# Kernel tuning notes

Hardware: AMD Instinct MI355X
Metric: run time of the kernel (lower is better)

Reference implementation:

```python
import jax, jax.numpy as jnp
import numpy as np

E = 8          # num_experts
H = 2048       # hidden_size
D = 4096       # expert_dim
R = 8          # lora rank
SCALE = 16.0 / 8.0  # lora_alpha / r
T = 2048       # tokens per expert


def setup_inputs() -> dict:
    key = jax.random.key(0)
    ks = jax.random.split(key, 7)
    s = lambda *shape: 1.0 / np.sqrt(shape[-1])
    hidden_states = jax.random.normal(ks[0], (E * T, H), dtype=jnp.float32)
    # base weights (nn.Linear convention: [out, in]) stacked over experts
    W_gu = jax.random.normal(ks[1], (E, 2 * D, H), dtype=jnp.float32) * s(H)
    W_d = jax.random.normal(ks[2], (E, H, D), dtype=jnp.float32) * s(D)
    # LoRA factors: A [r, in] (kaiming-ish), B [out, r] (zeros in training init;
    # use small random here so the delta path is exercised)
    A_gu = jax.random.normal(ks[3], (E, R, H), dtype=jnp.float32) * s(H)
    B_gu = jax.random.normal(ks[4], (E, 2 * D, R), dtype=jnp.float32) * 0.01
    A_d = jax.random.normal(ks[5], (E, R, D), dtype=jnp.float32) * s(D)
    B_d = jax.random.normal(ks[6], (E, H, R), dtype=jnp.float32) * 0.01
    return {"hidden_states": hidden_states, "W_gu": W_gu, "A_gu": A_gu,
            "B_gu": B_gu, "W_d": W_d, "A_d": A_d, "B_d": B_d}


def _lora_linear(x, W, A, B):
    # x: [e, t, in]; W: [e, out, in]; A: [e, r, in]; B: [e, out, r]
    base = jnp.einsum('eti,eoi->eto', x, W)
    low = jnp.einsum('eti,eri->etr', x, A)        # skinny projection
    delta = jnp.einsum('etr,eor->eto', low, B)
    return base + SCALE * delta


def reference(hidden_states, W_gu, A_gu, B_gu, W_d, A_d, B_d):
    x = hidden_states.reshape(E, -1, H)           # [E, T, H]
    gate_up = _lora_linear(x, W_gu, A_gu, B_gu)   # [E, T, 2D]
    gate, up = gate_up[..., :D], gate_up[..., D:]
    h = up * jax.nn.silu(gate)                    # SwiGLU [E, T, D]
    out = _lora_linear(h, W_d, A_d, B_d)          # [E, T, H]
    return out.reshape(-1, H)
```

## Files before the change

### kernel.cpp

```cpp
#include <hip/hip_runtime.h>
#include <hip/hip_bf16.h>

#define E_ 8
#define H_ 2048
#define D_ 4096
#define R_ 8
#define T_ 2048
#define TWO_D_ 8192
#define SCALE_ 2.0f

typedef __attribute__((ext_vector_type(8))) short short8;
typedef __attribute__((ext_vector_type(4))) float f32x4;

__device__ __forceinline__ unsigned short f2bf(float f) {
  union { float f; unsigned u; } c; c.f = f;
  unsigned u = c.u + 0x7fffu + ((c.u >> 16) & 1u);
  return (unsigned short)(u >> 16);
}

__device__ __forceinline__ void gl16(const void* g, void* l) {
  __builtin_amdgcn_global_load_lds(
      (const __attribute__((address_space(1))) void*)g,
      (__attribute__((address_space(3))) void*)l, 16, 0, 0);
}

__device__ __forceinline__ int lds_off(int rr, int ks, int lq) {
  return (((rr >> 5) & 3) << 13) | (((rr >> 7) & 1) << 12) | ((rr & 31) << 7) | (ks << 6) | (lq << 4);
}

__global__ __launch_bounds__(256) void k_pre(const float* __restrict__ x,
                                             unsigned short* __restrict__ xb,
                                             const float* __restrict__ Wgu,
                                             const float* __restrict__ Agu,
                                             const float* __restrict__ Bgu,
                                             unsigned short* __restrict__ wgub,
                                             const float* __restrict__ Wd,
                                             const float* __restrict__ Ad,
                                             const float* __restrict__ Bd,
                                             unsigned short* __restrict__ wdb) {
  const int NB_X = 1024, NB_GU = 8192;
  int bb = blockIdx.x, tid = threadIdx.x;
  if (bb < NB_X) {
    const long n = (long)E_ * T_ * H_;
    long i = ((long)bb * 256 + tid) * 8;
    const long stride = (long)NB_X * 256 * 8;
    for (; i < n; i += stride) {
      f32x4 a = *(const f32x4*)(x + i);
      f32x4 b = *(const f32x4*)(x + i + 4);
      ushort4 lo, hi;
      lo.x=f2bf(a[0]); lo.y=f2bf(a[1]); lo.z=f2bf(a[2]); lo.w=f2bf(a[3]);
      hi.x=f2bf(b[0]); hi.y=f2bf(b[1]); hi.z=f2bf(b[2]); hi.w=f2bf(b[3]);
      *(ushort4*)(xb + i) = lo;
      *(ushort4*)(xb + i + 4) = hi;
    }
  } else if (bb < NB_X + NB_GU) {
    int b2 = bb - NB_X;
    int e = b2 >> 10;
    int o8 = (b2 & 1023) * 8;
    int c = tid * 8;
    f32x4 a0[8], a1[8];
    #pragma unroll
    for (int r = 0; r < 8; ++r) {
      const float* ap = Agu + ((long)e * R_ + r) * H_ + c;
      a0[r] = *(const f32x4*)ap;
      a1[r] = *(const f32x4*)(ap + 4);
    }
    #pragma unroll
    for (int o = 0; o < 8; ++o) {
      long row = (long)e * TWO_D_ + o8 + o;
      const float* bp = Bgu + row * R_;
      const float* wp = Wgu + row * (long)H_ + c;
      f32x4 w0 = *(const f32x4*)wp;
      f32x4 w1 = *(const f32x4*)(wp + 4);
      #pragma unroll
      for (int r = 0; r < 8; ++r) {
        float s = SCALE_ * bp[r];
        w0 += s * a0[r];
        w1 += s * a1[r];
      }
      ushort4 lo, hi;
      lo.x=f2bf(w0[0]); lo.y=f2bf(w0[1]); lo.z=f2bf(w0[2]); lo.w=f2bf(w0[3]);
      hi.x=f2bf(w1[0]); hi.y=f2bf(w1[1]); hi.z=f2bf(w1[2]); hi.w=f2bf(w1[3]);
      unsigned short* op = wgub + row * (long)H_ + c;
      *(ushort4*)op = lo;
      *(ushort4*)(op + 4) = hi;
    }
  } else {
    int b2 = bb - NB_X - NB_GU;
    int e = b2 >> 9;
    int rem = b2 & 511;
    int h8 = (rem >> 1) * 8;
    int c = (rem & 1) * 2048 + tid * 8;
    f32x4 a0[8], a1[8];
    #pragma unroll
    for (int r = 0; r < 8; ++r) {
      const float* ap = Ad + ((long)e * R_ + r) * D_ + c;
      a0[r] = *(const f32x4*)ap;
      a1[r] = *(const f32x4*)(ap + 4);
    }
    #pragma unroll
    for (int o = 0; o < 8; ++o) {
      long row = (long)e * H_ + h8 + o;
      const float* bp = Bd + row * R_;
      const float* wp = Wd + row * (long)D_ + c;
      f32x4 w0 = *(const f32x4*)wp;
      f32x4 w1 = *(const f32x4*)(wp + 4);
      #pragma unroll
      for (int r = 0; r < 8; ++r) {
        float s = SCALE_ * bp[r];
        w0 += s * a0[r];
        w1 += s * a1[r];
      }
      ushort4 lo, hi;
      lo.x=f2bf(w0[0]); lo.y=f2bf(w0[1]); lo.z=f2bf(w0[2]); lo.w=f2bf(w0[3]);
      hi.x=f2bf(w1[0]); hi.y=f2bf(w1[1]); hi.z=f2bf(w1[2]); hi.w=f2bf(w1[3]);
      unsigned short* op = wdb + row * (long)D_ + c;
      *(ushort4*)op = lo;
      *(ushort4*)(op + 4) = hi;
    }
  }
}

__global__ __launch_bounds__(512, 2) void k_gemm1_8p(
    const unsigned short* __restrict__ Xb, const unsigned short* __restrict__ Wb,
    unsigned short* __restrict__ Hout) {
  __shared__ __align__(16) char lds[131072];

  const int MT = T_ / 256, NT = D_ / 128;
  int b = blockIdx.x;
  int cpx = (int)gridDim.x >> 3;
  int swz = (b & 7) * cpx + (b >> 3);
  int e  = swz / (MT * NT);
  int r0 = swz % (MT * NT);
  int nt = r0 / MT, mt = r0 % MT;

  int tid = threadIdx.x, lane = tid & 63;
  int wid = tid >> 6, wm = wid >> 2, wn = wid & 3;
  int lrow = lane & 15, lq = lane >> 4;
  int X4 = (lrow & 7) << 4;
  const int NKT = H_ / 64;

  unsigned ro = (unsigned)tid * 16;
  unsigned so = ro ^ (((ro >> 7) & 7u) << 4);
  int sh = (so >> 12) & 1, sr = (so >> 7) & 31, sc = (so & 127) >> 1;
  const unsigned short* pA[4]; const unsigned short* pB[4];
  #pragma unroll
  for (int q = 0; q < 4; ++q) {
    long arow = (long)e * T_ + mt * 256 + sh * 128 + q * 32 + sr;
    pA[q] = Xb + arow * H_ + sc;
    long wrow = sh ? ((long)e * TWO_D_ + D_ + nt * 128 + q * 32 + sr)
                   : ((long)e * TWO_D_ +      nt * 128 + q * 32 + sr);
    pB[q] = Wb + wrow * (long)H_ + sc;
  }
  auto SA = [&](int d, int q) { gl16(pA[q], lds + d * 32768 + q * 8192 + ro); pA[q] += 64; };
  auto SB = [&](int d, int q) { gl16(pB[q], lds + 65536 + d * 32768 + q * 8192 + ro); pB[q] += 64; };

  f32x4 accg[2][8] = {}, accu[2][8] = {};
  short8 BG[2][2], BU[2][2], af[2][2];

  SA(0,0); SB(0,0); SA(0,1); SB(0,1); SA(0,2); SB(0,2); SA(0,3); SB(0,3);
  SA(1,0); SB(1,0); SA(1,1); SB(1,1); SA(1,2); SB(1,2);
  asm volatile("s_waitcnt vmcnt(6)" ::: "memory");
  __builtin_amdgcn_s_barrier();

  int rbA = wm * 128 + lrow;
  for (int t = 0; t < NKT; ++t) {
    int d = t & 1;
    const char* Ab = lds + d * 32768;
    const char* Bb = lds + 65536 + d * 32768;

#define G1_MFMA(q)                                                                   \
    __builtin_amdgcn_s_setprio(1);                                                   \
    _Pragma("unroll") for (int m2 = 0; m2 < 2; ++m2)                                 \
      _Pragma("unroll") for (int ks = 0; ks < 2; ++ks)                               \
        _Pragma("unroll") for (int nj = 0; nj < 2; ++nj) {                           \
          accg[nj][(q)*2+m2] = __builtin_amdgcn_mfma_f32_16x16x32_bf16(              \
              BG[nj][ks], af[m2][ks], accg[nj][(q)*2+m2], 0, 0, 0);                  \
          accu[nj][(q)*2+m2] = __builtin_amdgcn_mfma_f32_16x16x32_bf16(              \
              BU[nj][ks], af[m2][ks], accu[nj][(q)*2+m2], 0, 0, 0);                  \
        }                                                                            \
    __builtin_amdgcn_s_setprio(0);

#define G1_LDA(q)                                                                    \
    _Pragma("unroll") for (int m2 = 0; m2 < 2; ++m2)                                 \
      _Pragma("unroll") for (int ks = 0; ks < 2; ++ks)                               \
        af[m2][ks] = *(const short8*)(Ab + (lds_off(rbA + ((q)*2+m2)*16, ks, lq) ^ X4));

#define G1_SYNC()                                                                    \
    __builtin_amdgcn_s_barrier();                                                    \
    asm volatile("s_waitcnt lgkmcnt(0)" ::: "memory");

    #pragma unroll
    for (int nj = 0; nj < 2; ++nj)
      #pragma unroll
      for (int ks = 0; ks < 2; ++ks) {
        int rg = wn * 32 + nj * 16 + lrow;
        BG[nj][ks] = *(const short8*)(Bb + (lds_off(rg, ks, lq) ^ X4));
        BU[nj][ks] = *(const short8*)(Bb + (lds_off(rg + 128, ks, lq) ^ X4));
      }
    G1_LDA(0);
    if (t + 1 < NKT) { SA(d ^ 1, 3); SB(d ^ 1, 3); }
    G1_SYNC();
    G1_MFMA(0);
    __builtin_amdgcn_s_barrier();
    G1_LDA(1);
    if (t + 2 < NKT) { SA(d, 0); SB(d, 0); }
    G1_SYNC();
    G1_MFMA(1);
    __builtin_amdgcn_s_barrier();
    G1_LDA(2);
    if (t + 2 < NKT) { SA(d, 1); SB(d, 1); }
    G1_SYNC();
    G1_MFMA(2);
    __builtin_amdgcn_s_barrier();
    G1_LDA(3);
    if (t + 2 < NKT) {
      SA(d, 2); SB(d, 2);
      asm volatile("s_waitcnt vmcnt(6)" ::: "memory");
    } else {
      asm volatile("s_waitcnt vmcnt(0)" ::: "memory");
    }
    G1_SYNC();
    G1_MFMA(3);
    __builtin_amdgcn_s_barrier();
  }

  __syncthreads();
  unsigned short* sT = (unsigned short*)(lds + 32768);
  #pragma unroll
  for (int mi = 0; mi < 8; ++mi) {
    int tl = rbA + mi * 16;
    #pragma unroll
    for (int nj = 0; nj < 2; ++nj) {
      int cb = wn * 32 + nj * 16 + lq * 4;
      ushort4 o;
      #pragma unroll
      for (int j = 0; j < 4; ++j) {
        float gate = accg[nj][mi][j];
        float up   = accu[nj][mi][j];
        float hh = up * (gate / (1.f + __expf(-gate)));
        (&o.x)[j] = f2bf(hh);
      }
      *(ushort4*)(sT + tl * 136 + cb) = o;
    }
  }
  __syncthreads();
  {
    long base = ((long)e * T_ + mt * 256) * D_ + nt * 128;
    int rr2 = tid >> 4, cc2 = (tid & 15) * 8;
    #pragma unroll
    for (int p = 0; p < 8; ++p) {
      int r = p * 32 + rr2;
      short8 v = *(const short8*)(sT + r * 136 + cc2);
      *(short8*)(Hout + base + (long)r * D_ + cc2) = v;
    }
  }
}

__global__ __launch_bounds__(512, 2) void k_gemm2_8p(
    const unsigned short* __restrict__ Hin, const unsigned short* __restrict__ Wdb,
    float* __restrict__ Out) {
  __shared__ __align__(16) char lds[131072];

  const int MT = T_ / 256, NT = H_ / 256;
  int b = blockIdx.x;
  int cpx = (int)gridDim.x >> 3;
  int swz = (b & 7) * cpx + (b >> 3);
  int e  = swz / (MT * NT);
  int r0 = swz % (MT * NT);
  int nt = r0 / MT, mt = r0 % MT;

  int tid = threadIdx.x, lane = tid & 63;
  int wid = tid >> 6, wm = wid >> 2, wn = wid & 3;
  int lrow = lane & 15, lq = lane >> 4;
  int X4 = (lrow & 7) << 4;
  const int NKT = D_ / 64;

  unsigned ro = (unsigned)tid * 16;
  unsigned so = ro ^ (((ro >> 7) & 7u) << 4);
  int sh = (so >> 12) & 1, sr = (so >> 7) & 31, sc = (so & 127) >> 1;
  const unsigned short* pA[4]; const unsigned short* pB[4];
  #pragma unroll
  for (int q = 0; q < 4; ++q) {
    long arow = (long)e * T_ + mt * 256 + sh * 128 + q * 32 + sr;
    pA[q] = Hin + arow * D_ + sc;
    long wrow = (long)e * H_ + nt * 256 + sh * 128 + q * 32 + sr;
    pB[q] = Wdb + wrow * (long)D_ + sc;
  }
  auto SA = [&](int d, int q) { gl16(pA[q], lds + d * 32768 + q * 8192 + ro); pA[q] += 64; };
  auto SB = [&](int d, int q) { gl16(pB[q], lds + 65536 + d * 32768 + q * 8192 + ro); pB[q] += 64; };

  f32x4 acc[8][4] = {};
  short8 BF[4][2], af[2][2];

  SA(0,0); SB(0,0); SA(0,1); SB(0,1); SA(0,2); SB(0,2); SA(0,3); SB(0,3);
  SA(1,0); SB(1,0); SA(1,1); SB(1,1); SA(1,2); SB(1,2);
  asm volatile("s_waitcnt vmcnt(6)" ::: "memory");
  __builtin_amdgcn_s_barrier();

  int rbA = wm * 128 + lrow;
  for (int t = 0; t < NKT; ++t) {
    int d = t & 1;
    const char* Ab = lds + d * 32768;
    const char* Bb = lds + 65536 + d * 32768;

#define G2_MFMA(q)                                                                   \
    __builtin_amdgcn_s_setprio(1);                                                   \
    _Pragma("unroll") for (int m2 = 0; m2 < 2; ++m2)                                 \
      _Pragma("unroll") for (int ks = 0; ks < 2; ++ks)                               \
        _Pragma("unroll") for (int ni = 0; ni < 4; ++ni)                             \
          acc[(q)*2+m2][ni] = __builtin_amdgcn_mfma_f32_16x16x32_bf16(               \
              af[m2][ks], BF[ni][ks], acc[(q)*2+m2][ni], 0, 0, 0);                   \
    __builtin_amdgcn_s_setprio(0);

#define G2_LDA(q)                                                                    \
    _Pragma("unroll") for (int m2 = 0; m2 < 2; ++m2)                                 \
      _Pragma("unroll") for (int ks = 0; ks < 2; ++ks)                               \
        af[m2][ks] = *(const short8*)(Ab + (lds_off(rbA + ((q)*2+m2)*16, ks, lq) ^ X4));

#define G2_SYNC()                                                                    \
    __builtin_amdgcn_s_barrier();                                                    \
    asm volatile("s_waitcnt lgkmcnt(0)" ::: "memory");

    #pragma unroll
    for (int ni = 0; ni < 4; ++ni)
      #pragma unroll
      for (int ks = 0; ks < 2; ++ks)
        BF[ni][ks] = *(const short8*)(Bb + (lds_off(wn * 64 + ni * 16 + lrow, ks, lq) ^ X4));
    G2_LDA(0);
    if (t + 1 < NKT) { SA(d ^ 1, 3); SB(d ^ 1, 3); }
    G2_SYNC();
    G2_MFMA(0);
    __builtin_amdgcn_s_barrier();
    G2_LDA(1);
    if (t + 2 < NKT) { SA(d, 0); SB(d, 0); }
    G2_SYNC();
    G2_MFMA(1);
    __builtin_amdgcn_s_barrier();
    G2_LDA(2);
    if (t + 2 < NKT) { SA(d, 1); SB(d, 1); }
    G2_SYNC();
    G2_MFMA(2);
    __builtin_amdgcn_s_barrier();
    G2_LDA(3);
    if (t + 2 < NKT) {
      SA(d, 2); SB(d, 2);
      asm volatile("s_waitcnt vmcnt(6)" ::: "memory");
    } else {
      asm volatile("s_waitcnt vmcnt(0)" ::: "memory");
    }
    G2_SYNC();
    G2_MFMA(3);
    __builtin_amdgcn_s_barrier();
  }

  {
    long rowbase = (long)e * T_ + mt * 256 + wm * 128;
    int colbase = nt * 256 + wn * 64;
    #pragma unroll
    for (int mi = 0; mi < 8; ++mi)
      #pragma unroll
      for (int j = 0; j < 4; ++j) {
        long row = rowbase + mi * 16 + lq * 4 + j;
        #pragma unroll
        for (int ni = 0; ni < 4; ++ni)
          Out[row * H_ + colbase + ni * 16 + lrow] = acc[mi][ni][j];
      }
  }
}

extern "C" void kernel_launch(void* const* d_in, const int* in_sizes, int n_in,
                              void* d_out, int out_size, void* d_ws, size_t ws_size,
                              hipStream_t stream) {
  const float* x   = (const float*)d_in[0];
  const float* Wgu = (const float*)d_in[1];
  const float* Agu = (const float*)d_in[2];
  const float* Bgu = (const float*)d_in[3];
  const float* Wd  = (const float*)d_in[4];
  const float* Ad  = (const float*)d_in[5];
  const float* Bd  = (const float*)d_in[6];
  float* out = (float*)d_out;

  char* ws = (char*)d_ws;
  const size_t SZ_H   = (size_t)E_ * T_ * D_ * 2;
  const size_t SZ_LOW = (size_t)E_ * T_ * R_ * 4;
  const size_t SZ_XB  = (size_t)E_ * T_ * H_ * 2;
  const size_t SZ_WGU = (size_t)E_ * TWO_D_ * H_ * 2;

  unsigned short* hbuf = (unsigned short*)ws;
  unsigned short* xb   = (unsigned short*)(ws + SZ_H + 2 * SZ_LOW);
  unsigned short* wgub = (unsigned short*)(ws + SZ_H + 2 * SZ_LOW + SZ_XB);
  unsigned short* wdb  = (unsigned short*)(ws + SZ_H + 2 * SZ_LOW + SZ_XB + SZ_WGU);

  hipLaunchKernelGGL(k_pre, dim3(1024 + 8192 + 4096), dim3(256), 0, stream,
                     x, xb, Wgu, Agu, Bgu, wgub, Wd, Ad, Bd, wdb);
  hipLaunchKernelGGL(k_gemm1_8p, dim3(E_ * (T_ / 256) * (D_ / 128)), dim3(512), 0, stream,
                     xb, wgub, hbuf);
  hipLaunchKernelGGL(k_gemm2_8p, dim3(E_ * (T_ / 256) * (H_ / 256)), dim3(512), 0, stream,
                     hbuf, wdb, out);
}
```

Before: 1.003 ms.

## Move down-proj weight merge into gemm1 grid to overlap with GEMM work

```diff
diff --git a/kernel.cpp b/kernel.cpp
--- a/kernel.cpp
+++ b/kernel.cpp
@@ -33,12 +33,8 @@
                                              const float* __restrict__ Wgu,
                                              const float* __restrict__ Agu,
                                              const float* __restrict__ Bgu,
-                                             unsigned short* __restrict__ wgub,
-                                             const float* __restrict__ Wd,
-                                             const float* __restrict__ Ad,
-                                             const float* __restrict__ Bd,
-                                             unsigned short* __restrict__ wdb) {
-  const int NB_X = 1024, NB_GU = 8192;
+                                             unsigned short* __restrict__ wgub) {
+  const int NB_X = 1024;
   int bb = blockIdx.x, tid = threadIdx.x;
   if (bb < NB_X) {
     const long n = (long)E_ * T_ * H_;
@@ -53,7 +49,7 @@
       *(ushort4*)(xb + i) = lo;
       *(ushort4*)(xb + i + 4) = hi;
     }
-  } else if (bb < NB_X + NB_GU) {
+  } else {
     int b2 = bb - NB_X;
     int e = b2 >> 10;
     int o8 = (b2 & 1023) * 8;
@@ -85,12 +81,21 @@
       *(ushort4*)op = lo;
       *(ushort4*)(op + 4) = hi;
     }
-  } else {
-    int b2 = bb - NB_X - NB_GU;
-    int e = b2 >> 9;
-    int rem = b2 & 511;
-    int h8 = (rem >> 1) * 8;
-    int c = (rem & 1) * 2048 + tid * 8;
+  }
+}
+
+__global__ __launch_bounds__(512, 2) void k_gemm1_8p(
+    const unsigned short* __restrict__ Xb, const unsigned short* __restrict__ Wb,
+    unsigned short* __restrict__ Hout,
+    const float* __restrict__ Wd, const float* __restrict__ Ad,
+    const float* __restrict__ Bd, unsigned short* __restrict__ wdb) {
+  const int NBG = 2048;
+  if ((int)blockIdx.x >= NBG) {
+    int b2 = blockIdx.x - NBG;
+    int tid = threadIdx.x;
+    int e = b2 >> 7;
+    int h16 = (b2 & 127) * 16;
+    int c = tid * 8;
     f32x4 a0[8], a1[8];
     #pragma unroll
     for (int r = 0; r < 8; ++r) {
@@ -98,9 +103,8 @@
       a0[r] = *(const f32x4*)ap;
       a1[r] = *(const f32x4*)(ap + 4);
     }
-    #pragma unroll
-    for (int o = 0; o < 8; ++o) {
-      long row = (long)e * H_ + h8 + o;
+    for (int o = 0; o < 16; ++o) {
+      long row = (long)e * H_ + h16 + o;
       const float* bp = Bd + row * R_;
       const float* wp = Wd + row * (long)D_ + c;
       f32x4 w0 = *(const f32x4*)wp;
@@ -118,17 +122,14 @@
       *(ushort4*)op = lo;
       *(ushort4*)(op + 4) = hi;
     }
-  }
-}
-
-__global__ __launch_bounds__(512, 2) void k_gemm1_8p(
-    const unsigned short* __restrict__ Xb, const unsigned short* __restrict__ Wb,
-    unsigned short* __restrict__ Hout) {
+    return;
+  }
+
   __shared__ __align__(16) char lds[131072];
 
   const int MT = T_ / 256, NT = D_ / 128;
   int b = blockIdx.x;
-  int cpx = (int)gridDim.x >> 3;
+  int cpx = NBG >> 3;
   int swz = (b & 7) * cpx + (b >> 3);
   int e  = swz / (MT * NT);
   int r0 = swz % (MT * NT);
@@ -392,10 +393,10 @@
   unsigned short* wgub = (unsigned short*)(ws + SZ_H + 2 * SZ_LOW + SZ_XB);
   unsigned short* wdb  = (unsigned short*)(ws + SZ_H + 2 * SZ_LOW + SZ_XB + SZ_WGU);
 
-  hipLaunchKernelGGL(k_pre, dim3(1024 + 8192 + 4096), dim3(256), 0, stream,
-                     x, xb, Wgu, Agu, Bgu, wgub, Wd, Ad, Bd, wdb);
-  hipLaunchKernelGGL(k_gemm1_8p, dim3(E_ * (T_ / 256) * (D_ / 128)), dim3(512), 0, stream,
-                     xb, wgub, hbuf);
+  hipLaunchKernelGGL(k_pre, dim3(1024 + 8192), dim3(256), 0, stream,
+                     x, xb, Wgu, Agu, Bgu, wgub);
+  hipLaunchKernelGGL(k_gemm1_8p, dim3(2048 + 1024), dim3(512), 0, stream,
+                     xb, wgub, hbuf, Wd, Ad, Bd, wdb);
   hipLaunchKernelGGL(k_gemm2_8p, dim3(E_ * (T_ / 256) * (H_ / 256)), dim3(512), 0, stream,
                      hbuf, wdb, out);
 }
```

Result: faster. 979.0 us (-2.4%).
